# Performance work log

Hardware: AMD Instinct MI355X
Metric: run time of the kernel (lower is better)

The kernel has to match this reference:

```python
import jax, jax.numpy as jnp
import numpy as np

D_MODEL = 1024
NUM_HEADS = 16
D_K = D_MODEL // NUM_HEADS  # 64
THETA = 10000.0
B, S = 2, 2048


def _rope(x, cos, sin):
    # x: [b, h, s, d]; cos/sin: [s, d//2] (broadcast over b, h)
    x1 = x[..., 0::2]
    x2 = x[..., 1::2]
    y1 = x1 * cos - x2 * sin
    y2 = x1 * sin + x2 * cos
    # interleave back: stack on last dim then flatten pairs
    return jnp.stack([y1, y2], axis=-1).reshape(x.shape)


def setup_inputs() -> dict:
    key = jax.random.key(0)
    ks = jax.random.split(key, 5)
    scale = 1.0 / np.sqrt(D_MODEL)
    return {
        "x": jax.random.normal(ks[0], (B, S, D_MODEL), dtype=jnp.float32),
        "token_positions": jnp.arange(S, dtype=jnp.int32),
        "Wq": jax.random.normal(ks[1], (D_MODEL, D_MODEL), dtype=jnp.float32) * scale,
        "Wk": jax.random.normal(ks[2], (D_MODEL, D_MODEL), dtype=jnp.float32) * scale,
        "Wv": jax.random.normal(ks[3], (D_MODEL, D_MODEL), dtype=jnp.float32) * scale,
        "Wo": jax.random.normal(ks[4], (D_MODEL, D_MODEL), dtype=jnp.float32) * scale,
    }


def reference(x, token_positions, Wq, Wk, Wv, Wo):
    b, s, _ = x.shape
    # torch nn.Linear semantics (no bias in this repo's Linear): y = x @ W.T
    q = jnp.einsum("bsd,od->bso", x, Wq)
    k = jnp.einsum("bsd,od->bso", x, Wk)
    v = jnp.einsum("bsd,od->bso", x, Wv)
    # split heads: b s (h d) -> b h s d
    def split(t):
        return t.reshape(b, s, NUM_HEADS, D_K).transpose(0, 2, 1, 3)
    q, k, v = split(q), split(k), split(v)

    # RoPE tables
    inv_freq = 1.0 / (THETA ** (jnp.arange(0, D_K, 2, dtype=jnp.float32) / D_K))  # [d/2]
    freqs = token_positions.astype(jnp.float32)[:, None] * inv_freq[None, :]      # [s, d/2]
    cos, sin = jnp.cos(freqs), jnp.sin(freqs)
    q = _rope(q, cos, sin)
    k = _rope(k, cos, sin)

    scale = D_K ** (-0.5)
    scores = jnp.einsum("bhqd,bhkd->bhqk", q, k) * scale  # [b,h,s,s]
    causal = jnp.tril(jnp.ones((s, s), dtype=bool))
    scores = jnp.where(causal, scores, -jnp.inf)
    attn = jax.nn.softmax(scores, axis=-1)
    out = jnp.einsum("bhqk,bhkd->bhqd", attn, v)
    out = out.transpose(0, 2, 1, 3).reshape(b, s, D_MODEL)  # b h s d -> b s (h d)
    return jnp.einsum("bsd,od->bso", out, Wo)
```

## Files before the change

### kernel.cpp

```cpp
#include <hip/hip_runtime.h>
#include <hip/hip_bf16.h>
#include <math.h>

#define SS 2048

typedef __attribute__((ext_vector_type(8))) __bf16 bf16x8;
typedef __attribute__((ext_vector_type(4))) float f32x4;
typedef __attribute__((ext_vector_type(16))) float f32x16;
typedef __attribute__((ext_vector_type(4))) unsigned int u32x4;
typedef __attribute__((ext_vector_type(4))) unsigned short u16x4;

__device__ __forceinline__ f32x4 mfma16(bf16x8 a, bf16x8 b, f32x4 c) {
  return __builtin_amdgcn_mfma_f32_16x16x32_bf16(a, b, c, 0, 0, 0);
}
__device__ __forceinline__ f32x16 mfma32(bf16x8 a, bf16x8 b, f32x16 c) {
  return __builtin_amdgcn_mfma_f32_32x32x16_bf16(a, b, c, 0, 0, 0);
}

__device__ __forceinline__ void gld_lds16(const void* g, void* l) {
  __builtin_amdgcn_global_load_lds(
      (__attribute__((address_space(1))) void*)(g),
      (__attribute__((address_space(3))) void*)(l), 16, 0, 0);
}

#if __has_builtin(__builtin_amdgcn_exp2f)
#define EXP2F(x) __builtin_amdgcn_exp2f(x)
#else
#define EXP2F(x) __expf(0.69314718056f * (x))
#endif

__device__ __forceinline__ unsigned int cvtpk_bf16(float lo, float hi) {
  unsigned int r;
  asm("v_cvt_pk_bf16_f32 %0, %1, %2" : "=v"(r) : "v"(lo), "v"(hi));
  return r;
}
__device__ __forceinline__ void swap32(unsigned int& x, unsigned int& y) {
  asm("v_permlane32_swap_b32 %0, %1" : "+v"(x), "+v"(y));
}
__device__ __forceinline__ unsigned short bfu(float v) {
  __bf16 h = (__bf16)v;
  return __builtin_bit_cast(unsigned short, h);
}

__global__ void prep_kernel(const float* __restrict__ x, const float* __restrict__ Wq,
                            const float* __restrict__ Wk, const float* __restrict__ Wv,
                            const float* __restrict__ Wo, const int* __restrict__ pos,
                            __bf16* __restrict__ xb, __bf16* __restrict__ Wb,
                            float2* __restrict__ tab) {
  const int bid = blockIdx.x, tid = threadIdx.x;
  if (bid >= 4096) {
    int i = (bid - 4096) * 256 + tid;
    int s = i >> 5, j = i & 31;
    float p = (float)pos[s];
    float inv = exp2f((float)j * -0.41524101186098283f);
    float f = p * inv;
    float sn, cs;
    sincosf(f, &sn, &cs);
    tab[i] = make_float2(cs, sn);
    return;
  }
  const float* s;
  __bf16* d;
  size_t base;
  if (bid < 2048) { s = x; d = xb; base = bid; }
  else {
    int seg = (bid - 2048) >> 9;
    s = (seg == 0) ? Wq : (seg == 1) ? Wk : (seg == 2) ? Wv : Wo;
    d = Wb + (size_t)seg * 1024 * 1024;
    base = (bid - 2048) & 511;
  }
  size_t i = (base * 256 + tid) * 8;
  float4 a = *reinterpret_cast<const float4*>(s + i);
  float4 b = *reinterpret_cast<const float4*>(s + i + 4);
  bf16x8 o;
  o[0] = (__bf16)a.x; o[1] = (__bf16)a.y; o[2] = (__bf16)a.z; o[3] = (__bf16)a.w;
  o[4] = (__bf16)b.x; o[5] = (__bf16)b.y; o[6] = (__bf16)b.z; o[7] = (__bf16)b.w;
  *reinterpret_cast<bf16x8*>(d + i) = o;
}

__global__ __launch_bounds__(512, 1) void gemm256_kernel(
    const __bf16* __restrict__ A, const __bf16* __restrict__ Bw,
    __bf16* __restrict__ C, __bf16* __restrict__ Vt,
    const float2* __restrict__ tab) {
  const int K = 1024, N = 3072, nk = 32;
  __shared__ __align__(16) __bf16 sm[65536];
  __bf16* lsA = sm;
  __bf16* lsB = sm + 32768;

  const int tid = threadIdx.x;
  const int lane = tid & 63;
  const int wave = tid >> 6;
  const int wr = wave >> 2, wc = wave & 3;

  const int xcd = blockIdx.x & 7;
  const int ii = blockIdx.x >> 3;
  const int m0 = (2 * xcd + (ii & 1)) * 256;
  const int n0 = (ii >> 1) * 256;

  const f32x4 fzero = {0.f, 0.f, 0.f, 0.f};
  f32x4 acc[8][4];
#pragma unroll
  for (int f = 0; f < 8; ++f)
#pragma unroll
    for (int g = 0; g < 4; ++g) acc[f][g] = fzero;

  const int srow = tid >> 2, schunk = tid & 3;
  const int ssc = schunk ^ ((srow >> 1) & 3);
  const __bf16* gA = A + (size_t)(m0 + srow) * K + ssc * 8;
  const __bf16* gB = Bw + (size_t)(n0 + srow) * K + ssc * 8;
  const size_t half128 = (size_t)128 * K;

#define STAGE256(kt_)                                              \
  do {                                                             \
    const int kc_ = (kt_) & 3;                                     \
    const __bf16* ga_ = gA + (size_t)(kt_) * 32;                   \
    const __bf16* gb_ = gB + (size_t)(kt_) * 32;                   \
    gld_lds16(ga_, lsA + kc_ * 8192 + tid * 8);                    \
    gld_lds16(ga_ + half128, lsA + kc_ * 8192 + 4096 + tid * 8);   \
    gld_lds16(gb_, lsB + kc_ * 8192 + tid * 8);                    \
    gld_lds16(gb_ + half128, lsB + kc_ * 8192 + 4096 + tid * 8);   \
  } while (0)

  STAGE256(0);
  STAGE256(1);

  const int lrow = lane & 15, hi = lane >> 4;

#pragma unroll 1
  for (int kt = 0; kt < nk; ++kt) {
    const int ks = (kt & 3) * 8192;
    if (kt + 2 < nk) {
      STAGE256(kt + 2);
      asm volatile("s_waitcnt vmcnt(8)" ::: "memory");
    } else if (kt == nk - 2) {
      asm volatile("s_waitcnt vmcnt(4)" ::: "memory");
    } else {
      asm volatile("s_waitcnt vmcnt(0)" ::: "memory");
    }
    __builtin_amdgcn_s_barrier();

    bf16x8 bfr[4];
#pragma unroll
    for (int g = 0; g < 4; ++g) {
      const int r = wc * 64 + g * 16 + lrow;
      bfr[g] = *reinterpret_cast<const bf16x8*>(
          lsB + ks + r * 32 + ((hi ^ ((r >> 1) & 3)) * 8));
    }
    bf16x8 af[4];
#pragma unroll
    for (int f = 0; f < 4; ++f) {
      const int r = wr * 128 + f * 16 + lrow;
      af[f] = *reinterpret_cast<const bf16x8*>(
          lsA + ks + r * 32 + ((hi ^ ((r >> 1) & 3)) * 8));
    }
    __builtin_amdgcn_s_setprio(1);
#pragma unroll
    for (int f = 0; f < 4; ++f)
#pragma unroll
      for (int g = 0; g < 4; ++g) acc[f][g] = mfma16(af[f], bfr[g], acc[f][g]);
    __builtin_amdgcn_s_setprio(0);
#pragma unroll
    for (int f = 0; f < 4; ++f) {
      const int r = wr * 128 + (f + 4) * 16 + lrow;
      af[f] = *reinterpret_cast<const bf16x8*>(
          lsA + ks + r * 32 + ((hi ^ ((r >> 1) & 3)) * 8));
    }
    __builtin_amdgcn_s_setprio(1);
#pragma unroll
    for (int f = 0; f < 4; ++f)
#pragma unroll
      for (int g = 0; g < 4; ++g) acc[f + 4][g] = mfma16(af[f], bfr[g], acc[f + 4][g]);
    __builtin_amdgcn_s_setprio(0);
  }
#undef STAGE256

  const int crow = (lane >> 4) * 4, ccol = lane & 15;
  if (n0 < 2048) {
    const int par = ccol & 1;
#pragma unroll
    for (int f = 0; f < 8; ++f) {
#pragma unroll
      for (int t = 0; t < 4; ++t) {
        const int r = m0 + wr * 128 + f * 16 + crow + t;
        const int s = r & (SS - 1);
#pragma unroll
        for (int g = 0; g < 4; ++g) {
          const int c = n0 + wc * 64 + g * 16 + ccol;
          const int jj = (c >> 1) & 31;
          float2 cs = tab[(s << 5) | jj];
          float v = acc[f][g][t];
          float o = __shfl_xor(v, 1);
          float y = par ? fmaf(o, cs.y, v * cs.x) : fmaf(v, cs.x, -o * cs.y);
          C[(size_t)r * N + c] = (__bf16)y;
        }
      }
    }
  } else {
#pragma unroll
    for (int f = 0; f < 8; ++f) {
      const int r0 = m0 + wr * 128 + f * 16 + crow;
      const int bb = r0 >> 11, s0 = r0 & (SS - 1);
#pragma unroll
      for (int g = 0; g < 4; ++g) {
        const int c = n0 - 2048 + wc * 64 + g * 16 + ccol;
        const int hh = c >> 6, dd = c & 63;
        u16x4 pk;
#pragma unroll
        for (int t = 0; t < 4; ++t) pk[t] = bfu(acc[f][g][t]);
        *reinterpret_cast<u16x4*>(Vt + ((size_t)(bb * 16 + hh) * 64 + dd) * SS + s0) = pk;
      }
    }
  }
}

template <typename OutT>
__global__ __launch_bounds__(256) void gemm_bt_kernel(
    const __bf16* __restrict__ A, const __bf16* __restrict__ Bw,
    OutT* __restrict__ C, int MT, int N, int K) {
  __shared__ __align__(16) __bf16 lA[2][128 * 32];
  __shared__ __align__(16) __bf16 lB[2][128 * 32];
  const int tid = threadIdx.x;
  const int lane = tid & 63;
  const int wave = tid >> 6;
  const int wr = wave >> 1, wc = wave & 1;

  const int cpx = (int)gridDim.x >> 3;
  const int flat = blockIdx.x;
  const int wg = (flat & 7) * cpx + (flat >> 3);
  const int MB = MT >> 3;
  const int NT = (int)gridDim.x / MT;
  const int band = wg / (MB * NT);
  const int inner = wg % (MB * NT);
  const int m0 = (band * MB + (inner % MB)) * 128;
  const int n0 = (inner / MB) * 128;

  const f32x4 fzero = {0.f, 0.f, 0.f, 0.f};
  f32x4 acc[4][4];
#pragma unroll
  for (int i = 0; i < 4; ++i)
#pragma unroll
    for (int j = 0; j < 4; ++j) acc[i][j] = fzero;

  const int srow = tid >> 2, scol = (tid & 3) * 8;
  const __bf16* gA = A + (size_t)(m0 + srow) * K + scol;
  const __bf16* gB = Bw + (size_t)(n0 + srow) * K + scol;
  const size_t half = (size_t)64 * K;
  const int lrow = lane & 15, lk8 = (lane >> 4) * 8;

  gld_lds16(gA, &lA[0][tid * 8]);
  gld_lds16(gA + half, &lA[0][tid * 8 + 2048]);
  gld_lds16(gB, &lB[0][tid * 8]);
  gld_lds16(gB + half, &lB[0][tid * 8 + 2048]);
  __syncthreads();

  const int nk = K >> 5;
  for (int t = 0; t < nk; ++t) {
    const int buf = t & 1;
    if (t + 1 < nk) {
      const int kt = (t + 1) * 32;
      gld_lds16(gA + kt, &lA[buf ^ 1][tid * 8]);
      gld_lds16(gA + kt + half, &lA[buf ^ 1][tid * 8 + 2048]);
      gld_lds16(gB + kt, &lB[buf ^ 1][tid * 8]);
      gld_lds16(gB + kt + half, &lB[buf ^ 1][tid * 8 + 2048]);
    }
    bf16x8 af[4], bfr[4];
#pragma unroll
    for (int i = 0; i < 4; ++i)
      af[i] = *reinterpret_cast<const bf16x8*>(&lA[buf][(wr * 64 + i * 16 + lrow) * 32 + lk8]);
#pragma unroll
    for (int j = 0; j < 4; ++j)
      bfr[j] = *reinterpret_cast<const bf16x8*>(&lB[buf][(wc * 64 + j * 16 + lrow) * 32 + lk8]);
    __builtin_amdgcn_s_setprio(1);
#pragma unroll
    for (int i = 0; i < 4; ++i)
#pragma unroll
      for (int j = 0; j < 4; ++j) acc[i][j] = mfma16(af[i], bfr[j], acc[i][j]);
    __builtin_amdgcn_s_setprio(0);
    __syncthreads();
  }

  const int crow = (lane >> 4) * 4, ccol = lane & 15;
#pragma unroll
  for (int i = 0; i < 4; ++i) {
#pragma unroll
    for (int j = 0; j < 4; ++j) {
      int r = m0 + wr * 64 + i * 16 + crow;
      int c = n0 + wc * 64 + j * 16 + ccol;
#pragma unroll
      for (int t = 0; t < 4; ++t) C[(size_t)(r + t) * N + c] = (OutT)acc[i][j][t];
    }
  }
}

#define CEXP 0.18033688011112042f
#define DMAX_THR 11.541560327111708f

__global__ __launch_bounds__(128) void attn_kernel(const __bf16* __restrict__ qkv,
                                                   const __bf16* __restrict__ Vt,
                                                   __bf16* __restrict__ AO) {
  const int bid = blockIdx.x;
  const int g = bid >> 8, c = bid & 255;
  const int b = c >> 7, h = (c >> 3) & 15, low = c & 7;
  const int qt = (g == 0) ? low : (g == 1) ? 31 - low : (g == 2) ? 15 - low : 16 + low;

  const int tid = threadIdx.x;
  const int wave = tid >> 6, lane = tid & 63;
  const int q32 = lane & 31, hi = lane >> 5;
  const int qw0 = qt * 64 + wave * 32;
  const int q = qw0 + q32;

  __shared__ __align__(16) __bf16 smem[16384];
  __bf16* lK0 = smem;
  __bf16* lV0 = smem + 8192;

  bf16x8 qb[4];
  {
    const __bf16* qr = qkv + (size_t)(b * SS + q) * 3072 + h * 64;
#pragma unroll
    for (int slot = 0; slot < 4; ++slot)
      qb[slot] = *reinterpret_cast<const bf16x8*>(qr + slot * 16 + hi * 8);
  }

  const __bf16* kbase = qkv + (size_t)(b * SS) * 3072 + 1024 + h * 64;
  const __bf16* vbase = Vt + (size_t)((b * 16 + h) * 64) * SS;

  const int srow = tid >> 3, scg = tid & 7;
  const int ssc = 8 * (scg ^ (srow & 7));
  const __bf16* kG0 = kbase + (size_t)srow * 3072 + ssc;
  const __bf16* vG0 = vbase + (size_t)srow * SS + ssc;

#define STAGE(buf_, kt_)                                                      \
  do {                                                                        \
    const __bf16* kG = kG0 + (size_t)(kt_)*64 * 3072;                         \
    const __bf16* vG = vG0 + (size_t)(kt_)*64;                                \
    _Pragma("unroll") for (int u = 0; u < 4; ++u) {                           \
      gld_lds16(kG + (size_t)u * 16 * 3072, lK0 + (buf_)*4096 + tid * 8 + u * 1024); \
      gld_lds16(vG + (size_t)u * 16 * SS, lV0 + (buf_)*4096 + tid * 8 + u * 1024);   \
    }                                                                         \
  } while (0)

  f32x16 o0 = {0,0,0,0,0,0,0,0,0,0,0,0,0,0,0,0};
  f32x16 o1 = {0,0,0,0,0,0,0,0,0,0,0,0,0,0,0,0};
  float mB = -INFINITY, lsum = 0.f;

  const int nkt = qt + 1;
  STAGE(0, 0);
  __syncthreads();

  for (int kt = 0; kt < nkt; ++kt) {
    const int buf = kt & 1;
    const int kvb = kt * 64;
    if (kt + 1 < nkt) STAGE(buf ^ 1, kt + 1);

    const __bf16* lk = lK0 + buf * 4096;
    const __bf16* lv = lV0 + buf * 4096;

    f32x16 s0 = {0,0,0,0,0,0,0,0,0,0,0,0,0,0,0,0};
    f32x16 s1 = {0,0,0,0,0,0,0,0,0,0,0,0,0,0,0,0};
    __builtin_amdgcn_s_setprio(1);
#pragma unroll
    for (int slot = 0; slot < 4; ++slot) {
      const int swz = 8 * ((slot * 2 + hi) ^ (q32 & 7));
      bf16x8 k0 = *reinterpret_cast<const bf16x8*>(lk + q32 * 64 + swz);
      bf16x8 k1 = *reinterpret_cast<const bf16x8*>(lk + (32 + q32) * 64 + swz);
      s0 = mfma32(k0, qb[slot], s0);
      s1 = mfma32(k1, qb[slot], s1);
    }
    __builtin_amdgcn_s_setprio(0);

    if (kt == qt) {
#pragma unroll
      for (int r = 0; r < 16; ++r) {
        const int rowc = (r & 3) + 8 * (r >> 2) + 4 * hi;
        if (kvb + rowc > q) s0[r] = -INFINITY;
        if (kvb + 32 + rowc > q) s1[r] = -INFINITY;
      }
    }

    float pm = s0[0];
#pragma unroll
    for (int r = 1; r < 16; ++r) pm = fmaxf(pm, s0[r]);
#pragma unroll
    for (int r = 0; r < 16; ++r) pm = fmaxf(pm, s1[r]);
    pm = fmaxf(pm, __shfl_xor(pm, 32));
    const float pmB = pm * CEXP;
    if (!__all(pmB <= mB + DMAX_THR)) {
      const float mnB = fmaxf(mB, pmB);
      const float alpha = EXP2F(mB - mnB);
      mB = mnB;
      lsum *= alpha;
#pragma unroll
      for (int r = 0; r < 16; ++r) { o0[r] *= alpha; o1[r] *= alpha; }
    }
    float rs = 0.f;
#pragma unroll
    for (int r = 0; r < 16; ++r) { s0[r] = EXP2F(fmaf(s0[r], CEXP, -mB)); rs += s0[r]; }
#pragma unroll
    for (int r = 0; r < 16; ++r) { s1[r] = EXP2F(fmaf(s1[r], CEXP, -mB)); rs += s1[r]; }
    rs += __shfl_xor(rs, 32);
    lsum += rs;

    bf16x8 pb[4];
    {
      unsigned int A = cvtpk_bf16(s0[0], s0[1]), B2 = cvtpk_bf16(s0[2], s0[3]);
      unsigned int C2 = cvtpk_bf16(s0[4], s0[5]), D2 = cvtpk_bf16(s0[6], s0[7]);
      swap32(A, C2); swap32(B2, D2);
      u32x4 t0 = {A, B2, C2, D2};
      pb[0] = __builtin_bit_cast(bf16x8, t0);
      unsigned int E = cvtpk_bf16(s0[8], s0[9]), F = cvtpk_bf16(s0[10], s0[11]);
      unsigned int G = cvtpk_bf16(s0[12], s0[13]), H = cvtpk_bf16(s0[14], s0[15]);
      swap32(E, G); swap32(F, H);
      u32x4 t1 = {E, F, G, H};
      pb[1] = __builtin_bit_cast(bf16x8, t1);
      unsigned int A3 = cvtpk_bf16(s1[0], s1[1]), B3 = cvtpk_bf16(s1[2], s1[3]);
      unsigned int C3 = cvtpk_bf16(s1[4], s1[5]), D3 = cvtpk_bf16(s1[6], s1[7]);
      swap32(A3, C3); swap32(B3, D3);
      u32x4 t2 = {A3, B3, C3, D3};
      pb[2] = __builtin_bit_cast(bf16x8, t2);
      unsigned int E3 = cvtpk_bf16(s1[8], s1[9]), F3 = cvtpk_bf16(s1[10], s1[11]);
      unsigned int G3 = cvtpk_bf16(s1[12], s1[13]), H3 = cvtpk_bf16(s1[14], s1[15]);
      swap32(E3, G3); swap32(F3, H3);
      u32x4 t3 = {E3, F3, G3, H3};
      pb[3] = __builtin_bit_cast(bf16x8, t3);
    }

    __builtin_amdgcn_s_setprio(1);
#pragma unroll
    for (int slot = 0; slot < 4; ++slot) {
      const int swz = 8 * ((slot * 2 + hi) ^ (q32 & 7));
      bf16x8 v0 = *reinterpret_cast<const bf16x8*>(lv + q32 * 64 + swz);
      bf16x8 v1 = *reinterpret_cast<const bf16x8*>(lv + (32 + q32) * 64 + swz);
      o0 = mfma32(v0, pb[slot], o0);
      o1 = mfma32(v1, pb[slot], o1);
    }
    __builtin_amdgcn_s_setprio(0);

    __syncthreads();
  }

  const float inv = 1.0f / lsum;
  __bf16* ol = smem + wave * 2304;
#pragma unroll
  for (int r = 0; r < 16; ++r) {
    const int d = (r & 3) + 8 * (r >> 2) + 4 * hi;
    ol[q32 * 72 + d] = (__bf16)(o0[r] * inv);
    ol[q32 * 72 + 32 + d] = (__bf16)(o1[r] * inv);
  }
#pragma unroll
  for (int pass = 0; pass < 4; ++pass) {
    const int idx = pass * 64 + lane;
    const int row = idx >> 3, colc = idx & 7;
    bf16x8 v = *reinterpret_cast<const bf16x8*>(ol + row * 72 + colc * 8);
    *reinterpret_cast<bf16x8*>(
        AO + (size_t)(b * SS + qt * 64 + wave * 32 + row) * 1024 + h * 64 + colc * 8) = v;
  }
#undef STAGE
}

extern "C" void kernel_launch(void* const* d_in, const int* in_sizes, int n_in,
                              void* d_out, int out_size, void* d_ws, size_t ws_size,
                              hipStream_t stream) {
  const float* x  = (const float*)d_in[0];
  const int* pos  = (const int*)d_in[1];
  const float* Wq = (const float*)d_in[2];
  const float* Wk = (const float*)d_in[3];
  const float* Wv = (const float*)d_in[4];
  const float* Wo = (const float*)d_in[5];

  __bf16* xb  = (__bf16*)d_ws;
  __bf16* Wb  = xb + (size_t)4096 * 1024;
  __bf16* qkv = Wb + (size_t)4096 * 1024;
  __bf16* Vt  = qkv + (size_t)4096 * 3072;
  __bf16* ao  = Vt + (size_t)2048 * 2048;
  float2* tab = (float2*)(ao + (size_t)4096 * 1024);

  prep_kernel<<<4352, 256, 0, stream>>>(x, Wq, Wk, Wv, Wo, pos, xb, Wb, tab);

  gemm256_kernel<<<192, 512, 0, stream>>>(xb, Wb, qkv, Vt, tab);
  attn_kernel<<<1024, 128, 0, stream>>>(qkv, Vt, ao);
  gemm_bt_kernel<float><<<256, 256, 0, stream>>>(
      ao, Wb + (size_t)3 * 1024 * 1024, (float*)d_out, 32, 1024, 1024);
}
```

Baseline: 117.5 us.

## Use single-wave attention blocks processing 64 query rows per wave

```diff
diff --git a/kernel.cpp b/kernel.cpp
--- a/kernel.cpp
+++ b/kernel.cpp
@@ -295,76 +295,141 @@
 #define CEXP 0.18033688011112042f
 #define DMAX_THR 11.541560327111708f
 
-__global__ __launch_bounds__(128) void attn_kernel(const __bf16* __restrict__ qkv,
-                                                   const __bf16* __restrict__ Vt,
-                                                   __bf16* __restrict__ AO) {
+#define MAXRED(S0, S1, PM)                                                  \
+  float PM;                                                                 \
+  {                                                                         \
+    float t0_ = fmaxf(fmaxf(S0[0], S0[8]), fmaxf(S1[0], S1[8]));            \
+    float t1_ = fmaxf(fmaxf(S0[1], S0[9]), fmaxf(S1[1], S1[9]));            \
+    float t2_ = fmaxf(fmaxf(S0[2], S0[10]), fmaxf(S1[2], S1[10]));          \
+    float t3_ = fmaxf(fmaxf(S0[3], S0[11]), fmaxf(S1[3], S1[11]));          \
+    float t4_ = fmaxf(fmaxf(S0[4], S0[12]), fmaxf(S1[4], S1[12]));          \
+    float t5_ = fmaxf(fmaxf(S0[5], S0[13]), fmaxf(S1[5], S1[13]));          \
+    float t6_ = fmaxf(fmaxf(S0[6], S0[14]), fmaxf(S1[6], S1[14]));          \
+    float t7_ = fmaxf(fmaxf(S0[7], S0[15]), fmaxf(S1[7], S1[15]));          \
+    PM = fmaxf(fmaxf(fmaxf(t0_, t1_), fmaxf(t2_, t3_)),                     \
+               fmaxf(fmaxf(t4_, t5_), fmaxf(t6_, t7_)));                    \
+    PM = fmaxf(PM, __shfl_xor(PM, 32));                                     \
+    PM *= CEXP;                                                             \
+  }
+
+#define EXPSUM(S0, S1, M, L)                                                \
+  {                                                                         \
+    float a0_ = 0.f, a1_ = 0.f, a2_ = 0.f, a3_ = 0.f;                       \
+    _Pragma("unroll") for (int r = 0; r < 16; r += 4) {                     \
+      S0[r] = EXP2F(fmaf(S0[r], CEXP, -(M))); a0_ += S0[r];                 \
+      S0[r + 1] = EXP2F(fmaf(S0[r + 1], CEXP, -(M))); a1_ += S0[r + 1];     \
+      S0[r + 2] = EXP2F(fmaf(S0[r + 2], CEXP, -(M))); a2_ += S0[r + 2];     \
+      S0[r + 3] = EXP2F(fmaf(S0[r + 3], CEXP, -(M))); a3_ += S0[r + 3];     \
+    }                                                                       \
+    _Pragma("unroll") for (int r = 0; r < 16; r += 4) {                     \
+      S1[r] = EXP2F(fmaf(S1[r], CEXP, -(M))); a0_ += S1[r];                 \
+      S1[r + 1] = EXP2F(fmaf(S1[r + 1], CEXP, -(M))); a1_ += S1[r + 1];     \
+      S1[r + 2] = EXP2F(fmaf(S1[r + 2], CEXP, -(M))); a2_ += S1[r + 2];     \
+      S1[r + 3] = EXP2F(fmaf(S1[r + 3], CEXP, -(M))); a3_ += S1[r + 3];     \
+    }                                                                       \
+    float rs_ = (a0_ + a1_) + (a2_ + a3_);                                  \
+    rs_ += __shfl_xor(rs_, 32);                                             \
+    L += rs_;                                                               \
+  }
+
+#define CVTPB(S0, S1, PB)                                                   \
+  {                                                                         \
+    unsigned int A_ = cvtpk_bf16(S0[0], S0[1]), B_ = cvtpk_bf16(S0[2], S0[3]); \
+    unsigned int C_ = cvtpk_bf16(S0[4], S0[5]), D_ = cvtpk_bf16(S0[6], S0[7]); \
+    swap32(A_, C_); swap32(B_, D_);                                         \
+    u32x4 t0_ = {A_, B_, C_, D_};                                           \
+    PB[0] = __builtin_bit_cast(bf16x8, t0_);                                \
+    unsigned int E_ = cvtpk_bf16(S0[8], S0[9]), F_ = cvtpk_bf16(S0[10], S0[11]); \
+    unsigned int G_ = cvtpk_bf16(S0[12], S0[13]), H_ = cvtpk_bf16(S0[14], S0[15]); \
+    swap32(E_, G_); swap32(F_, H_);                                         \
+    u32x4 t1_ = {E_, F_, G_, H_};                                           \
+    PB[1] = __builtin_bit_cast(bf16x8, t1_);                                \
+    unsigned int I_ = cvtpk_bf16(S1[0], S1[1]), J_ = cvtpk_bf16(S1[2], S1[3]); \
+    unsigned int K_ = cvtpk_bf16(S1[4], S1[5]), L_ = cvtpk_bf16(S1[6], S1[7]); \
+    swap32(I_, K_); swap32(J_, L_);                                         \
+    u32x4 t2_ = {I_, J_, K_, L_};                                           \
+    PB[2] = __builtin_bit_cast(bf16x8, t2_);                                \
+    unsigned int M_ = cvtpk_bf16(S1[8], S1[9]), N_ = cvtpk_bf16(S1[10], S1[11]); \
+    unsigned int O_ = cvtpk_bf16(S1[12], S1[13]), P_ = cvtpk_bf16(S1[14], S1[15]); \
+    swap32(M_, O_); swap32(N_, P_);                                         \
+    u32x4 t3_ = {M_, N_, O_, P_};                                           \
+    PB[3] = __builtin_bit_cast(bf16x8, t3_);                                \
+  }
+
+__global__ __launch_bounds__(64) void attn_kernel(const __bf16* __restrict__ qkv,
+                                                  const __bf16* __restrict__ Vt,
+                                                  __bf16* __restrict__ AO) {
   const int bid = blockIdx.x;
   const int g = bid >> 8, c = bid & 255;
   const int b = c >> 7, h = (c >> 3) & 15, low = c & 7;
   const int qt = (g == 0) ? low : (g == 1) ? 31 - low : (g == 2) ? 15 - low : 16 + low;
 
-  const int tid = threadIdx.x;
-  const int wave = tid >> 6, lane = tid & 63;
+  const int lane = threadIdx.x;
   const int q32 = lane & 31, hi = lane >> 5;
-  const int qw0 = qt * 64 + wave * 32;
-  const int q = qw0 + q32;
-
-  __shared__ __align__(16) __bf16 smem[16384];
-  __bf16* lK0 = smem;
-  __bf16* lV0 = smem + 8192;
-
-  bf16x8 qb[4];
+  const int qA = qt * 64 + q32;
+
+  __shared__ __align__(16) __bf16 smem[2][8192];
+
+  bf16x8 qfA[4], qfB[4];
   {
-    const __bf16* qr = qkv + (size_t)(b * SS + q) * 3072 + h * 64;
-#pragma unroll
-    for (int slot = 0; slot < 4; ++slot)
-      qb[slot] = *reinterpret_cast<const bf16x8*>(qr + slot * 16 + hi * 8);
-  }
+    const __bf16* qrA = qkv + (size_t)(b * SS + qA) * 3072 + h * 64;
+    const __bf16* qrB = qrA + (size_t)32 * 3072;
+#pragma unroll
+    for (int s = 0; s < 4; ++s) {
+      qfA[s] = *reinterpret_cast<const bf16x8*>(qrA + s * 16 + hi * 8);
+      qfB[s] = *reinterpret_cast<const bf16x8*>(qrB + s * 16 + hi * 8);
+    }
+  }
+  asm volatile("s_waitcnt vmcnt(0)" ::: "memory");
 
   const __bf16* kbase = qkv + (size_t)(b * SS) * 3072 + 1024 + h * 64;
   const __bf16* vbase = Vt + (size_t)((b * 16 + h) * 64) * SS;
-
-  const int srow = tid >> 3, scg = tid & 7;
-  const int ssc = 8 * (scg ^ (srow & 7));
-  const __bf16* kG0 = kbase + (size_t)srow * 3072 + ssc;
-  const __bf16* vG0 = vbase + (size_t)srow * SS + ssc;
-
-#define STAGE(buf_, kt_)                                                      \
+  const int sr = lane >> 3;
+  const int sc8 = 8 * ((lane & 7) ^ sr);
+  const __bf16* kG0 = kbase + (size_t)sr * 3072 + sc8;
+  const __bf16* vG0 = vbase + (size_t)sr * SS + sc8;
+
+#define STAGE(slot_, kt_)                                                     \
   do {                                                                        \
-    const __bf16* kG = kG0 + (size_t)(kt_)*64 * 3072;                         \
-    const __bf16* vG = vG0 + (size_t)(kt_)*64;                                \
-    _Pragma("unroll") for (int u = 0; u < 4; ++u) {                           \
-      gld_lds16(kG + (size_t)u * 16 * 3072, lK0 + (buf_)*4096 + tid * 8 + u * 1024); \
-      gld_lds16(vG + (size_t)u * 16 * SS, lV0 + (buf_)*4096 + tid * 8 + u * 1024);   \
+    const __bf16* kG_ = kG0 + (size_t)(kt_) * 64 * 3072;                      \
+    const __bf16* vG_ = vG0 + (size_t)(kt_) * 64;                             \
+    _Pragma("unroll") for (int u = 0; u < 8; ++u) {                           \
+      gld_lds16(kG_ + (size_t)u * 8 * 3072, &smem[slot_][u * 512 + lane * 8]); \
+      gld_lds16(vG_ + (size_t)u * 8 * SS, &smem[slot_][4096 + u * 512 + lane * 8]); \
     }                                                                         \
   } while (0)
 
-  f32x16 o0 = {0,0,0,0,0,0,0,0,0,0,0,0,0,0,0,0};
-  f32x16 o1 = {0,0,0,0,0,0,0,0,0,0,0,0,0,0,0,0};
-  float mB = -INFINITY, lsum = 0.f;
+  f32x16 oA0 = {0,0,0,0,0,0,0,0,0,0,0,0,0,0,0,0};
+  f32x16 oA1 = oA0, oB0 = oA0, oB1 = oA0;
+  float mA = -INFINITY, lsA = 0.f, mB = -INFINITY, lsB = 0.f;
 
   const int nkt = qt + 1;
   STAGE(0, 0);
-  __syncthreads();
-
+
+#pragma unroll 1
   for (int kt = 0; kt < nkt; ++kt) {
-    const int buf = kt & 1;
-    const int kvb = kt * 64;
-    if (kt + 1 < nkt) STAGE(buf ^ 1, kt + 1);
-
-    const __bf16* lk = lK0 + buf * 4096;
-    const __bf16* lv = lV0 + buf * 4096;
-
-    f32x16 s0 = {0,0,0,0,0,0,0,0,0,0,0,0,0,0,0,0};
-    f32x16 s1 = {0,0,0,0,0,0,0,0,0,0,0,0,0,0,0,0};
+    const int slot = kt & 1;
+    if (kt + 1 < nkt) {
+      STAGE(slot ^ 1, kt + 1);
+      asm volatile("s_waitcnt vmcnt(16)" ::: "memory");
+    } else {
+      asm volatile("s_waitcnt vmcnt(0)" ::: "memory");
+    }
+    const __bf16* lk = smem[slot];
+    const __bf16* lv = smem[slot] + 4096;
+
+    f32x16 sA0 = {0,0,0,0,0,0,0,0,0,0,0,0,0,0,0,0};
+    f32x16 sA1 = sA0, sB0 = sA0, sB1 = sA0;
     __builtin_amdgcn_s_setprio(1);
 #pragma unroll
-    for (int slot = 0; slot < 4; ++slot) {
-      const int swz = 8 * ((slot * 2 + hi) ^ (q32 & 7));
+    for (int s = 0; s < 4; ++s) {
+      const int swz = 8 * (((s << 1) | hi) ^ (q32 & 7));
       bf16x8 k0 = *reinterpret_cast<const bf16x8*>(lk + q32 * 64 + swz);
       bf16x8 k1 = *reinterpret_cast<const bf16x8*>(lk + (32 + q32) * 64 + swz);
-      s0 = mfma32(k0, qb[slot], s0);
-      s1 = mfma32(k1, qb[slot], s1);
+      sA0 = mfma32(k0, qfA[s], sA0);
+      sA1 = mfma32(k1, qfA[s], sA1);
+      sB0 = mfma32(k0, qfB[s], sB0);
+      sB1 = mfma32(k1, qfB[s], sB1);
     }
     __builtin_amdgcn_s_setprio(0);
 
@@ -372,89 +437,69 @@
 #pragma unroll
       for (int r = 0; r < 16; ++r) {
         const int rowc = (r & 3) + 8 * (r >> 2) + 4 * hi;
-        if (kvb + rowc > q) s0[r] = -INFINITY;
-        if (kvb + 32 + rowc > q) s1[r] = -INFINITY;
+        if (rowc > q32) sA0[r] = -INFINITY;
+        sA1[r] = -INFINITY;
+        if (rowc > q32) sB1[r] = -INFINITY;
       }
     }
 
-    float pm = s0[0];
-#pragma unroll
-    for (int r = 1; r < 16; ++r) pm = fmaxf(pm, s0[r]);
-#pragma unroll
-    for (int r = 0; r < 16; ++r) pm = fmaxf(pm, s1[r]);
-    pm = fmaxf(pm, __shfl_xor(pm, 32));
-    const float pmB = pm * CEXP;
-    if (!__all(pmB <= mB + DMAX_THR)) {
-      const float mnB = fmaxf(mB, pmB);
-      const float alpha = EXP2F(mB - mnB);
-      mB = mnB;
-      lsum *= alpha;
-#pragma unroll
-      for (int r = 0; r < 16; ++r) { o0[r] *= alpha; o1[r] *= alpha; }
-    }
-    float rs = 0.f;
-#pragma unroll
-    for (int r = 0; r < 16; ++r) { s0[r] = EXP2F(fmaf(s0[r], CEXP, -mB)); rs += s0[r]; }
-#pragma unroll
-    for (int r = 0; r < 16; ++r) { s1[r] = EXP2F(fmaf(s1[r], CEXP, -mB)); rs += s1[r]; }
-    rs += __shfl_xor(rs, 32);
-    lsum += rs;
-
-    bf16x8 pb[4];
-    {
-      unsigned int A = cvtpk_bf16(s0[0], s0[1]), B2 = cvtpk_bf16(s0[2], s0[3]);
-      unsigned int C2 = cvtpk_bf16(s0[4], s0[5]), D2 = cvtpk_bf16(s0[6], s0[7]);
-      swap32(A, C2); swap32(B2, D2);
-      u32x4 t0 = {A, B2, C2, D2};
-      pb[0] = __builtin_bit_cast(bf16x8, t0);
-      unsigned int E = cvtpk_bf16(s0[8], s0[9]), F = cvtpk_bf16(s0[10], s0[11]);
-      unsigned int G = cvtpk_bf16(s0[12], s0[13]), H = cvtpk_bf16(s0[14], s0[15]);
-      swap32(E, G); swap32(F, H);
-      u32x4 t1 = {E, F, G, H};
-      pb[1] = __builtin_bit_cast(bf16x8, t1);
-      unsigned int A3 = cvtpk_bf16(s1[0], s1[1]), B3 = cvtpk_bf16(s1[2], s1[3]);
-      unsigned int C3 = cvtpk_bf16(s1[4], s1[5]), D3 = cvtpk_bf16(s1[6], s1[7]);
-      swap32(A3, C3); swap32(B3, D3);
-      u32x4 t2 = {A3, B3, C3, D3};
-      pb[2] = __builtin_bit_cast(bf16x8, t2);
-      unsigned int E3 = cvtpk_bf16(s1[8], s1[9]), F3 = cvtpk_bf16(s1[10], s1[11]);
-      unsigned int G3 = cvtpk_bf16(s1[12], s1[13]), H3 = cvtpk_bf16(s1[14], s1[15]);
-      swap32(E3, G3); swap32(F3, H3);
-      u32x4 t3 = {E3, F3, G3, H3};
-      pb[3] = __builtin_bit_cast(bf16x8, t3);
-    }
+    MAXRED(sA0, sA1, pmA)
+    MAXRED(sB0, sB1, pmB)
+    if (!__all((pmA <= mA + DMAX_THR) && (pmB <= mB + DMAX_THR))) {
+      {
+        const float mn = fmaxf(mA, pmA);
+        const float al = EXP2F(mA - mn);
+        mA = mn; lsA *= al;
+#pragma unroll
+        for (int r = 0; r < 16; ++r) { oA0[r] *= al; oA1[r] *= al; }
+      }
+      {
+        const float mn = fmaxf(mB, pmB);
+        const float al = EXP2F(mB - mn);
+        mB = mn; lsB *= al;
+#pragma unroll
+        for (int r = 0; r < 16; ++r) { oB0[r] *= al; oB1[r] *= al; }
+      }
+    }
+    EXPSUM(sA0, sA1, mA, lsA)
+    EXPSUM(sB0, sB1, mB, lsB)
+
+    bf16x8 pbA[4], pbB[4];
+    CVTPB(sA0, sA1, pbA)
+    CVTPB(sB0, sB1, pbB)
 
     __builtin_amdgcn_s_setprio(1);
 #pragma unroll
-    for (int slot = 0; slot < 4; ++slot) {
-      const int swz = 8 * ((slot * 2 + hi) ^ (q32 & 7));
+    for (int s = 0; s < 4; ++s) {
+      const int swz = 8 * (((s << 1) | hi) ^ (q32 & 7));
       bf16x8 v0 = *reinterpret_cast<const bf16x8*>(lv + q32 * 64 + swz);
       bf16x8 v1 = *reinterpret_cast<const bf16x8*>(lv + (32 + q32) * 64 + swz);
-      o0 = mfma32(v0, pb[slot], o0);
-      o1 = mfma32(v1, pb[slot], o1);
+      oA0 = mfma32(v0, pbA[s], oA0);
+      oA1 = mfma32(v1, pbA[s], oA1);
+      oB0 = mfma32(v0, pbB[s], oB0);
+      oB1 = mfma32(v1, pbB[s], oB1);
     }
     __builtin_amdgcn_s_setprio(0);
-
-    __syncthreads();
-  }
-
-  const float inv = 1.0f / lsum;
-  __bf16* ol = smem + wave * 2304;
+  }
+#undef STAGE
+
+  const float invA = 1.0f / lsA, invB = 1.0f / lsB;
+  __bf16* ol = smem[0];
 #pragma unroll
   for (int r = 0; r < 16; ++r) {
     const int d = (r & 3) + 8 * (r >> 2) + 4 * hi;
-    ol[q32 * 72 + d] = (__bf16)(o0[r] * inv);
-    ol[q32 * 72 + 32 + d] = (__bf16)(o1[r] * inv);
-  }
-#pragma unroll
-  for (int pass = 0; pass < 4; ++pass) {
-    const int idx = pass * 64 + lane;
-    const int row = idx >> 3, colc = idx & 7;
+    ol[q32 * 72 + d] = (__bf16)(oA0[r] * invA);
+    ol[q32 * 72 + 32 + d] = (__bf16)(oA1[r] * invA);
+    ol[(32 + q32) * 72 + d] = (__bf16)(oB0[r] * invB);
+    ol[(32 + q32) * 72 + 32 + d] = (__bf16)(oB1[r] * invB);
+  }
+#pragma unroll
+  for (int pass = 0; pass < 8; ++pass) {
+    const int row = pass * 8 + (lane >> 3), colc = lane & 7;
     bf16x8 v = *reinterpret_cast<const bf16x8*>(ol + row * 72 + colc * 8);
     *reinterpret_cast<bf16x8*>(
-        AO + (size_t)(b * SS + qt * 64 + wave * 32 + row) * 1024 + h * 64 + colc * 8) = v;
-  }
-#undef STAGE
+        AO + (size_t)(b * SS + qt * 64 + row) * 1024 + h * 64 + colc * 8) = v;
+  }
 }
 
 extern "C" void kernel_launch(void* const* d_in, const int* in_sizes, int n_in,
@@ -475,9 +520,8 @@
   float2* tab = (float2*)(ao + (size_t)4096 * 1024);
 
   prep_kernel<<<4352, 256, 0, stream>>>(x, Wq, Wk, Wv, Wo, pos, xb, Wb, tab);
-
   gemm256_kernel<<<192, 512, 0, stream>>>(xb, Wb, qkv, Vt, tab);
-  attn_kernel<<<1024, 128, 0, stream>>>(qkv, Vt, ao);
+  attn_kernel<<<1024, 64, 0, stream>>>(qkv, Vt, ao);
   gemm_bt_kernel<float><<<256, 256, 0, stream>>>(
       ao, Wb + (size_t)3 * 1024 * 1024, (float*)d_out, 32, 1024, 1024);
 }
```

After: 138.7 us. 18.1% more time.
